# Performance work log

Measured on AMD Instinct MI355X. Metric: run time of the kernel, lower is better.

## Reference

```python
import jax, jax.numpy as jnp
import numpy as np

VOCAB, DIM, B, L, OUT = 100000, 50, 4096, 512, 20

def setup_inputs() -> dict:
    key = jax.random.key(0)
    k1, k2, k3, k4, k5 = jax.random.split(key, 5)
    x = jax.random.randint(k1, (B, L), 0, VOCAB, dtype=jnp.int64)
    lengths = jax.random.randint(k2, (B,), 1, L + 1, dtype=jnp.int64)  # at least 1 token
    emb_table = jax.random.normal(k3, (VOCAB, DIM), dtype=jnp.float32)
    W = jax.random.normal(k4, (OUT, DIM), dtype=jnp.float32) * 0.1
    b = jax.random.normal(k5, (OUT,), dtype=jnp.float32) * 0.1
    return {"x": x, "lengths": lengths, "emb_table": emb_table, "W": W, "b": b}

def reference(x, lengths, emb_table, W, b):
    # embedding gather: [B, L, D]
    emb = emb_table[x]
    # masked mean over the first lengths[i] tokens of each sample
    mask = (jnp.arange(emb.shape[1])[None, :] < lengths[:, None]).astype(emb.dtype)  # [B, L]
    denom = lengths.astype(emb.dtype)[:, None]                                        # [B, 1]
    rep = jnp.einsum('bld,bl->bd', emb, mask) / denom                                 # [B, D]
    rep = jax.nn.relu(rep)
    logits = rep @ W.T + b                                                            # [B, OUT]
    return logits
```

## Files before the change

kernel.cpp:

```cpp
#include <hip/hip_runtime.h>


#define LMAX 512
#define DIMV 50
#define OUTV 20

__global__ __launch_bounds__(256) void fused_embed_mean_linear(
    const int*   __restrict__ x,
    const int*   __restrict__ lengths,
    const float* __restrict__ emb,
    const float* __restrict__ W,
    const float* __restrict__ bias,
    float*       __restrict__ out)
{
    const int b    = blockIdx.x;
    const int tid  = threadIdx.x;
    const int wave = tid >> 6;
    const int lane = tid & 63;

    __shared__ int   sidx[LMAX];
    __shared__ float sacc[4][DIMV];
    __shared__ float srep[DIMV];

    const int len = lengths[b];

    const int xbase = b * LMAX;
    for (int i = tid; i < len; i += 256) sidx[i] = x[xbase + i];
    __syncthreads();

    if (lane < DIMV) {
        float acc0 = 0.f, acc1 = 0.f;
        int l = wave;
        for (; l + 28 < len; l += 32) {
            float v0 = emb[sidx[l      ] * DIMV + lane];
            float v1 = emb[sidx[l + 4  ] * DIMV + lane];
            float v2 = emb[sidx[l + 8  ] * DIMV + lane];
            float v3 = emb[sidx[l + 12 ] * DIMV + lane];
            float v4 = emb[sidx[l + 16 ] * DIMV + lane];
            float v5 = emb[sidx[l + 20 ] * DIMV + lane];
            float v6 = emb[sidx[l + 24 ] * DIMV + lane];
            float v7 = emb[sidx[l + 28 ] * DIMV + lane];
            acc0 += (v0 + v1) + (v2 + v3);
            acc1 += (v4 + v5) + (v6 + v7);
        }
        for (; l < len; l += 4)
            acc0 += emb[sidx[l] * DIMV + lane];
        sacc[wave][lane] = acc0 + acc1;
    }
    __syncthreads();

    if (tid < DIMV) {
        float s = sacc[0][tid] + sacc[1][tid] + sacc[2][tid] + sacc[3][tid];
        s /= (float)len;
        srep[tid] = fmaxf(s, 0.f);
    }
    __syncthreads();

    if (tid < OUTV) {
        float s = bias[tid];
        const float* wr = W + tid * DIMV;
        #pragma unroll
        for (int d = 0; d < DIMV; ++d) s += srep[d] * wr[d];
        out[b * OUTV + tid] = s;
    }
}

extern "C" void kernel_launch(void* const* d_in, const int* in_sizes, int n_in,
                              void* d_out, int out_size, void* d_ws, size_t ws_size,
                              hipStream_t stream) {
    const int*   x       = (const int*)  d_in[0];
    const int*   lengths = (const int*)  d_in[1];
    const float* emb     = (const float*)d_in[2];
    const float* W       = (const float*)d_in[3];
    const float* bias    = (const float*)d_in[4];
    float* out = (float*)d_out;

    const int B = in_sizes[1];
    fused_embed_mean_linear<<<B, 256, 0, stream>>>(x, lengths, emb, W, bias, out);
}
```

Baseline: 111.2 us.

## Convert embedding table to fp16 per call and gather half2 pairs

Adds a pre-pass kernel that converts the whole fp32 embedding table into fp16 in the workspace. The main kernel then gathers rows as half2, with two tokens handled per wave (32 lanes each) and the halves combined by a cross-lane shuffle. The aim is to halve the bytes moved by the random row gathers and fill more lanes per wave. In exchange it reads and writes the full 5M-element table every call, adds a second launch, and loses precision in the summed embeddings.

```diff
diff --git a/kernel.cpp b/kernel.cpp
--- a/kernel.cpp
+++ b/kernel.cpp
@@ -1,14 +1,31 @@
 #include <hip/hip_runtime.h>
+#include <hip/hip_fp16.h>
 
 
-#define LMAX 512
-#define DIMV 50
-#define OUTV 20
+#define LMAX   512
+#define DIMV   50
+#define OUTV   20
+#define VOCABSZ 100000
 
-__global__ __launch_bounds__(256) void fused_embed_mean_linear(
+__global__ __launch_bounds__(256) void cvt_table_f16(
+    const float* __restrict__ emb, __half* __restrict__ tab)
+{
+    const int i = (blockIdx.x * 256 + threadIdx.x) * 8;
+    if (i >= VOCABSZ * DIMV) return;
+    const float4 a = *reinterpret_cast<const float4*>(emb + i);
+    const float4 b = *reinterpret_cast<const float4*>(emb + i + 4);
+    __half2 h[4];
+    h[0] = __floats2half2_rn(a.x, a.y);
+    h[1] = __floats2half2_rn(a.z, a.w);
+    h[2] = __floats2half2_rn(b.x, b.y);
+    h[3] = __floats2half2_rn(b.z, b.w);
+    *reinterpret_cast<float4*>(tab + i) = *reinterpret_cast<const float4*>(h);
+}
+
+__global__ __launch_bounds__(256) void fused_embed_mean_linear_f16(
     const int*   __restrict__ x,
     const int*   __restrict__ lengths,
-    const float* __restrict__ emb,
+    const __half* __restrict__ tab,
     const float* __restrict__ W,
     const float* __restrict__ bias,
     float*       __restrict__ out)
@@ -17,10 +34,12 @@
     const int tid  = threadIdx.x;
     const int wave = tid >> 6;
     const int lane = tid & 63;
+    const int slot = lane >> 5;
+    const int j    = lane & 31;
 
-    __shared__ int   sidx[LMAX];
-    __shared__ float sacc[4][DIMV];
-    __shared__ float srep[DIMV];
+    __shared__ int    sidx[LMAX];
+    __shared__ float2 sacc[4][25];
+    __shared__ float  srep[DIMV];
 
     const int len = lengths[b];
 
@@ -28,31 +47,52 @@
     for (int i = tid; i < len; i += 256) sidx[i] = x[xbase + i];
     __syncthreads();
 
-    if (lane < DIMV) {
-        float acc0 = 0.f, acc1 = 0.f;
-        int l = wave;
-        for (; l + 28 < len; l += 32) {
-            float v0 = emb[sidx[l      ] * DIMV + lane];
-            float v1 = emb[sidx[l + 4  ] * DIMV + lane];
-            float v2 = emb[sidx[l + 8  ] * DIMV + lane];
-            float v3 = emb[sidx[l + 12 ] * DIMV + lane];
-            float v4 = emb[sidx[l + 16 ] * DIMV + lane];
-            float v5 = emb[sidx[l + 20 ] * DIMV + lane];
-            float v6 = emb[sidx[l + 24 ] * DIMV + lane];
-            float v7 = emb[sidx[l + 28 ] * DIMV + lane];
-            acc0 += (v0 + v1) + (v2 + v3);
-            acc1 += (v4 + v5) + (v6 + v7);
+    float2 acc0 = {0.f, 0.f}, acc1 = {0.f, 0.f};
+    if (j < 25) {
+        const int np = (len + 1) >> 1;
+        int p = wave;
+        for (; p + 28 < np; p += 32) {
+            #pragma unroll
+            for (int u = 0; u < 8; u += 2) {
+                const int ta = 2 * (p + 4 * u)       + slot;
+                const int tb = 2 * (p + 4 * (u + 1)) + slot;
+                float2 fa = {0.f, 0.f}, fb = {0.f, 0.f};
+                if (ta < len) {
+                    const __half2 h = *reinterpret_cast<const __half2*>(
+                        tab + sidx[ta] * DIMV + 2 * j);
+                    fa.x = __low2float(h); fa.y = __high2float(h);
+                }
+                if (tb < len) {
+                    const __half2 h = *reinterpret_cast<const __half2*>(
+                        tab + sidx[tb] * DIMV + 2 * j);
+                    fb.x = __low2float(h); fb.y = __high2float(h);
+                }
+                acc0.x += fa.x; acc0.y += fa.y;
+                acc1.x += fb.x; acc1.y += fb.y;
+            }
         }
-        for (; l < len; l += 4)
-            acc0 += emb[sidx[l] * DIMV + lane];
-        sacc[wave][lane] = acc0 + acc1;
+        for (; p < np; p += 4) {
+            const int t = 2 * p + slot;
+            if (t < len) {
+                const __half2 h = *reinterpret_cast<const __half2*>(
+                    tab + sidx[t] * DIMV + 2 * j);
+                acc0.x += __low2float(h); acc0.y += __high2float(h);
+            }
+        }
     }
+    acc0.x += acc1.x; acc0.y += acc1.y;
+    acc0.x += __shfl_down(acc0.x, 32);
+    acc0.y += __shfl_down(acc0.y, 32);
+    if (slot == 0 && j < 25) sacc[wave][j] = acc0;
     __syncthreads();
 
-    if (tid < DIMV) {
-        float s = sacc[0][tid] + sacc[1][tid] + sacc[2][tid] + sacc[3][tid];
-        s /= (float)len;
-        srep[tid] = fmaxf(s, 0.f);
+    if (tid < 25) {
+        float2 s = sacc[0][tid];
+        #pragma unroll
+        for (int w = 1; w < 4; ++w) { s.x += sacc[w][tid].x; s.y += sacc[w][tid].y; }
+        const float inv = 1.0f / (float)len;
+        srep[2 * tid]     = fmaxf(s.x * inv, 0.f);
+        srep[2 * tid + 1] = fmaxf(s.y * inv, 0.f);
     }
     __syncthreads();
 
@@ -73,8 +113,12 @@
     const float* emb     = (const float*)d_in[2];
     const float* W       = (const float*)d_in[3];
     const float* bias    = (const float*)d_in[4];
-    float* out = (float*)d_out;
+    float*  out = (float*)d_out;
+    __half* tab = (__half*)d_ws;
 
     const int B = in_sizes[1];
-    fused_embed_mean_linear<<<B, 256, 0, stream>>>(x, lengths, emb, W, bias, out);
+
+    const int nconv = (VOCABSZ * DIMV) / 8;
+    cvt_table_f16<<<(nconv + 255) / 256, 256, 0, stream>>>(emb, tab);
+    fused_embed_mean_linear_f16<<<B, 256, 0, stream>>>(x, lengths, tab, W, bias, out);
 }
```

Result: slower. 124.0 us (+11.5%).

## Convert embedding table to padded fp16 and gather 4 tokens per wave

Applied to the files above, without the earlier changes.

Adds a pre-pass that converts the fp32 embedding table to fp16 rows padded to 64 elements (128 bytes), with an extra zero row used as the padding index. The main kernel then gathers 8-byte chunks, one quarter-wave per token, so each wave loads four tokens per instruction, and reduces across quarter-waves with shuffles. Token slots past the length point at the zero row, so the tail needs no masking. This halves gather bytes and aligns rows, at the cost of rebuilding a ~13MB table on every call and losing precision to fp16 rounding.

```diff
diff --git a/kernel.cpp b/kernel.cpp
--- a/kernel.cpp
+++ b/kernel.cpp
@@ -1,58 +1,118 @@
 #include <hip/hip_runtime.h>
+#include <hip/hip_fp16.h>
 
 
-#define LMAX 512
-#define DIMV 50
-#define OUTV 20
+#define LMAX    512
+#define DIMV    50
+#define OUTV    20
+#define VOCABSZ 100000
+#define RSTRIDE 64
 
-__global__ __launch_bounds__(256) void fused_embed_mean_linear(
-    const int*   __restrict__ x,
-    const int*   __restrict__ lengths,
-    const float* __restrict__ emb,
-    const float* __restrict__ W,
-    const float* __restrict__ bias,
-    float*       __restrict__ out)
+struct __align__(8) H4 { __half2 a, b; };
+
+__global__ __launch_bounds__(256) void build_tab(
+    const float* __restrict__ emb, __half* __restrict__ tab)
+{
+    const int t = blockIdx.x * 256 + threadIdx.x;
+    const int r = t >> 4;
+    const int q = t & 15;
+    if (r > VOCABSZ) return;
+    float4 v = {0.f, 0.f, 0.f, 0.f};
+    if (r < VOCABSZ) {
+        const float* src = emb + r * DIMV + q * 4;
+        if (q < 12) {
+            float2 a = *reinterpret_cast<const float2*>(src);
+            float2 c = *reinterpret_cast<const float2*>(src + 2);
+            v.x = a.x; v.y = a.y; v.z = c.x; v.w = c.y;
+        } else if (q == 12) {
+            float2 a = *reinterpret_cast<const float2*>(src);
+            v.x = a.x; v.y = a.y;
+        }
+    }
+    H4 h;
+    h.a = __floats2half2_rn(v.x, v.y);
+    h.b = __floats2half2_rn(v.z, v.w);
+    *reinterpret_cast<H4*>(tab + r * RSTRIDE + q * 4) = h;
+}
+
+__device__ inline void accum(float4& a, const H4& h) {
+    float2 f0 = __half22float2(h.a);
+    float2 f1 = __half22float2(h.b);
+    a.x += f0.x; a.y += f0.y; a.z += f1.x; a.w += f1.y;
+}
+
+__global__ __launch_bounds__(256) void fused_gather(
+    const int*    __restrict__ x,
+    const int*    __restrict__ lengths,
+    const __half* __restrict__ tab,
+    const float*  __restrict__ W,
+    const float*  __restrict__ bias,
+    float*        __restrict__ out)
 {
     const int b    = blockIdx.x;
     const int tid  = threadIdx.x;
     const int wave = tid >> 6;
     const int lane = tid & 63;
+    const int rg   = lane >> 4;
+    const int cl   = lane & 15;
 
     __shared__ int   sidx[LMAX];
-    __shared__ float sacc[4][DIMV];
+    __shared__ float sacc[4][64];
     __shared__ float srep[DIMV];
 
     const int len = lengths[b];
 
     const int xbase = b * LMAX;
-    for (int i = tid; i < len; i += 256) sidx[i] = x[xbase + i];
+    #pragma unroll
+    for (int i = 0; i < LMAX; i += 256) {
+        const int ii = i + tid;
+        const int v  = x[xbase + ii];
+        sidx[ii] = (ii < len) ? v : VOCABSZ;
+    }
     __syncthreads();
 
-    if (lane < DIMV) {
-        float acc0 = 0.f, acc1 = 0.f;
-        int l = wave;
-        for (; l + 28 < len; l += 32) {
-            float v0 = emb[sidx[l      ] * DIMV + lane];
-            float v1 = emb[sidx[l + 4  ] * DIMV + lane];
-            float v2 = emb[sidx[l + 8  ] * DIMV + lane];
-            float v3 = emb[sidx[l + 12 ] * DIMV + lane];
-            float v4 = emb[sidx[l + 16 ] * DIMV + lane];
-            float v5 = emb[sidx[l + 20 ] * DIMV + lane];
-            float v6 = emb[sidx[l + 24 ] * DIMV + lane];
-            float v7 = emb[sidx[l + 28 ] * DIMV + lane];
-            acc0 += (v0 + v1) + (v2 + v3);
-            acc1 += (v4 + v5) + (v6 + v7);
-        }
-        for (; l < len; l += 4)
-            acc0 += emb[sidx[l] * DIMV + lane];
-        sacc[wave][lane] = acc0 + acc1;
+    const __half* tabc = tab + cl * 4;
+    const int nchunk = (len + 3) >> 2;
+    float4 acc = {0.f, 0.f, 0.f, 0.f};
+
+    int c = wave;
+    for (; c + 28 < nchunk; c += 32) {
+        int i0 = sidx[(c     ) * 4 + rg];
+        int i1 = sidx[(c +  4) * 4 + rg];
+        int i2 = sidx[(c +  8) * 4 + rg];
+        int i3 = sidx[(c + 12) * 4 + rg];
+        int i4 = sidx[(c + 16) * 4 + rg];
+        int i5 = sidx[(c + 20) * 4 + rg];
+        int i6 = sidx[(c + 24) * 4 + rg];
+        int i7 = sidx[(c + 28) * 4 + rg];
+        H4 h0 = *reinterpret_cast<const H4*>(tabc + (i0 << 6));
+        H4 h1 = *reinterpret_cast<const H4*>(tabc + (i1 << 6));
+        H4 h2 = *reinterpret_cast<const H4*>(tabc + (i2 << 6));
+        H4 h3 = *reinterpret_cast<const H4*>(tabc + (i3 << 6));
+        H4 h4 = *reinterpret_cast<const H4*>(tabc + (i4 << 6));
+        H4 h5 = *reinterpret_cast<const H4*>(tabc + (i5 << 6));
+        H4 h6 = *reinterpret_cast<const H4*>(tabc + (i6 << 6));
+        H4 h7 = *reinterpret_cast<const H4*>(tabc + (i7 << 6));
+        accum(acc, h0); accum(acc, h1); accum(acc, h2); accum(acc, h3);
+        accum(acc, h4); accum(acc, h5); accum(acc, h6); accum(acc, h7);
     }
+    for (; c < nchunk; c += 4) {
+        int i0 = sidx[c * 4 + rg];
+        H4 h0 = *reinterpret_cast<const H4*>(tabc + (i0 << 6));
+        accum(acc, h0);
+    }
+
+    acc.x += __shfl_xor(acc.x, 16); acc.y += __shfl_xor(acc.y, 16);
+    acc.z += __shfl_xor(acc.z, 16); acc.w += __shfl_xor(acc.w, 16);
+    acc.x += __shfl_xor(acc.x, 32); acc.y += __shfl_xor(acc.y, 32);
+    acc.z += __shfl_xor(acc.z, 32); acc.w += __shfl_xor(acc.w, 32);
+    if (lane < 16)
+        *reinterpret_cast<float4*>(&sacc[wave][lane * 4]) = acc;
     __syncthreads();
 
     if (tid < DIMV) {
         float s = sacc[0][tid] + sacc[1][tid] + sacc[2][tid] + sacc[3][tid];
-        s /= (float)len;
-        srep[tid] = fmaxf(s, 0.f);
+        srep[tid] = fmaxf(s / (float)len, 0.f);
     }
     __syncthreads();
 
@@ -73,8 +133,12 @@
     const float* emb     = (const float*)d_in[2];
     const float* W       = (const float*)d_in[3];
     const float* bias    = (const float*)d_in[4];
-    float* out = (float*)d_out;
+    float*  out = (float*)d_out;
+    __half* tab = (__half*)d_ws;
 
     const int B = in_sizes[1];
-    fused_embed_mean_linear<<<B, 256, 0, stream>>>(x, lengths, emb, W, bias, out);
+
+    const int nthr = (VOCABSZ + 1) * 16;
+    build_tab<<<(nthr + 255) / 256, 256, 0, stream>>>(emb, tab);
+    fused_gather<<<B, 256, 0, stream>>>(x, lengths, tab, W, bias, out);
 }
```

Measured after the change: 98.82 us. -11.1%, faster.
